# Performance work log

Hardware: AMD Instinct MI355X
Metric: run time of the kernel (lower is better)

The kernel has to match this reference:

```python
import jax, jax.numpy as jnp
import numpy as np

IN_F = 256
OUT_F = 256
ALPHA = 0.2  # LeakyReLU negative slope


def _xavier(key, shape, gain=1.414):
    fan_in, fan_out = shape[0], shape[1]
    limit = gain * np.sqrt(6.0 / (fan_in + fan_out))
    return jax.random.uniform(key, shape, jnp.float32, -limit, limit)


def setup_inputs() -> dict:
    key = jax.random.key(0)
    k1, k2, k3, k4, k5, k6 = jax.random.split(key, 6)
    B, N = 8, 2048
    h = jax.random.normal(k1, (B, N, IN_F), jnp.float32)
    adj = jax.random.randint(k2, (B, N, N), 0, 2, jnp.int32)
    lrgt1 = jax.random.normal(k3, (B, N, OUT_F), jnp.float32)
    W1 = _xavier(k4, (IN_F, IN_F))
    W2 = _xavier(k5, (OUT_F, OUT_F))
    a = _xavier(k6, (2 * IN_F, 1))
    return {"h": h, "adj": adj, "lrgt1": lrgt1, "W1": W1, "W2": W2, "a": a}


def reference(h, adj, lrgt1, W1, W2, a):
    # Wh: [B,N,in], wlrgt: [B,N,out]
    Wh = jnp.matmul(h, W1)
    wlrgt = jnp.matmul(lrgt1, W2)
    # additive attention scores: e[b,i,j] = leaky_relu(Wh_i @ a1 + Wh_j @ a2)
    a1 = a[:IN_F, 0]   # [in]
    a2 = a[IN_F:, 0]   # [in]
    Wh1 = jnp.einsum('bnc,c->bn', Wh, a1)  # [B,N]
    Wh2 = jnp.einsum('bnc,c->bn', Wh, a2)  # [B,N]
    e = jax.nn.leaky_relu(Wh1[:, :, None] + Wh2[:, None, :], ALPHA)  # [B,N,N]
    neg = jnp.float32(-9e15)
    masked = jnp.where(adj > 0, e, neg)
    attention = jax.nn.softmax(masked, axis=2)
    # dropout p=0.0 / eval mode -> identity
    h_prime = jnp.matmul(attention, Wh)      # [B,N,in]
    gt_prime = jnp.matmul(attention, wlrgt)  # [B,N,out]
    return (jax.nn.elu(h_prime), jax.nn.elu(gt_prime))
```

## Files before the change

kernel.cpp:

```cpp
#include <hip/hip_runtime.h>
#include <hip/hip_bf16.h>

#define IN_F 256
#define NN   2048
#define BB   8

typedef unsigned short u16;
typedef unsigned long long u64;
typedef __attribute__((ext_vector_type(8))) short short8x;
typedef __attribute__((ext_vector_type(4))) float float4x;

__device__ __forceinline__ u16 f2b(float f) {
    union { float f; unsigned int u; } x; x.f = f;
    unsigned int r = x.u + 0x7FFFu + ((x.u >> 16) & 1u);
    return (u16)(r >> 16);
}

__global__ __launch_bounds__(256) void adjpack(const int* __restrict__ adj,
                                               u64* __restrict__ mask)
{
    const int wid  = (blockIdx.x * 256 + threadIdx.x) >> 6;
    const int lane = threadIdx.x & 63;
#pragma unroll 4
    for (int it = 0; it < 64; ++it) {
        const long s = (long)it * 8192 + wid;
        const int v = __builtin_nontemporal_load(adj + s * 64 + lane);
        const u64 m = __ballot(v > 0);
        if (lane == 0) mask[s] = m;
    }
}

__device__ __forceinline__ void transp_body4(const float* __restrict__ src,
                                             u16* __restrict__ dst,
                                             int R, int C, int tid,
                                             float (*tile)[33])
{
    const int per = (R / 32) * (C / 32);
    const int b  = tid / per;
    const int tt = tid % per;
    const int jt = tt / (C / 32);
    const int ct = tt % (C / 32);
    src += (long)b * R * C;
    dst += (long)b * R * C;

    const int t = threadIdx.x;
    const int lr = t >> 3, lc = (t & 7) * 4;
    float4 v = *(const float4*)(src + (long)(jt * 32 + lr) * C + ct * 32 + lc);
    tile[lr][lc + 0] = v.x;
    tile[lr][lc + 1] = v.y;
    tile[lr][lc + 2] = v.z;
    tile[lr][lc + 3] = v.w;
    __syncthreads();
    const int c = t >> 3, r4 = (t & 7) * 4;
    ushort4 o;
    o.x = f2b(tile[r4 + 0][c]);
    o.y = f2b(tile[r4 + 1][c]);
    o.z = f2b(tile[r4 + 2][c]);
    o.w = f2b(tile[r4 + 3][c]);
    *(ushort4*)(dst + (long)(ct * 32 + c) * R + jt * 32 + r4) = o;
}

__global__ __launch_bounds__(256) void prep(const float* __restrict__ h,
                                            const float* __restrict__ g,
                                            const float* __restrict__ W1,
                                            const float* __restrict__ W2,
                                            const float* __restrict__ a,
                                            u16* __restrict__ HbfT,
                                            u16* __restrict__ GbfT,
                                            u16* __restrict__ W1T,
                                            u16* __restrict__ W2T,
                                            float* __restrict__ v1,
                                            float* __restrict__ v2)
{
    __shared__ float tile[32][33];
    __shared__ float s1[IN_F], s2[IN_F];
    const int bid = blockIdx.x;

    if (bid < 4096) {
        transp_body4(h, HbfT, NN, IN_F, bid, tile);
    } else if (bid < 8192) {
        transp_body4(g, GbfT, NN, IN_F, bid - 4096, tile);
    } else if (bid < 8256) {
        transp_body4(W1, W1T, IN_F, IN_F, bid - 8192, tile);
    } else if (bid < 8320) {
        transp_body4(W2, W2T, IN_F, IN_F, bid - 8256, tile);
    } else {
        const int t = threadIdx.x;
        s1[t] = a[t];
        s2[t] = a[IN_F + t];
        __syncthreads();
        float acc1 = 0.f, acc2 = 0.f;
        for (int c = 0; c < IN_F; ++c) {
            float w = W1[t * IN_F + c];
            acc1 += w * s1[c];
            acc2 += w * s2[c];
        }
        v1[t] = acc1;
        v2[t] = acc2;
    }
}

__global__ __launch_bounds__(256) void rowdots(const float* __restrict__ h,
                                               const float* __restrict__ v1,
                                               const float* __restrict__ v2,
                                               float* __restrict__ Wh1,
                                               float* __restrict__ Wh2)
{
    const int wave = threadIdx.x >> 6;
    const int lane = threadIdx.x & 63;
    const long row = (long)blockIdx.x * 4 + wave;
    const int c0 = lane * 4;

    float4 v  = *(const float4*)(h + row * IN_F + c0);
    float4 a1 = *(const float4*)(v1 + c0);
    float4 a2 = *(const float4*)(v2 + c0);

    float s1 = v.x * a1.x + v.y * a1.y + v.z * a1.z + v.w * a1.w;
    float s2 = v.x * a2.x + v.y * a2.y + v.z * a2.z + v.w * a2.w;
#pragma unroll
    for (int off = 32; off; off >>= 1) {
        s1 += __shfl_xor(s1, off, 64);
        s2 += __shfl_xor(s2, off, 64);
    }
    if (lane == 0) { Wh1[row] = s1; Wh2[row] = s2; }
}

#define AREAD(AR, KS)                                                         \
    _Pragma("unroll") for (int rt = 0; rt < 4; ++rt)                          \
        AR[rt] = *(const short8x*)&ab[((KS) * 4 + rt) * 512 + lane * 8];

#define MFMA16(AR, G)                                                         \
    _Pragma("unroll") for (int rt = 0; rt < 4; ++rt)                          \
        _Pragma("unroll") for (int ct = 0; ct < 4; ++ct)                      \
            acc[rt][ct] = __builtin_amdgcn_mfma_f32_16x16x32_bf16(AR[rt], G[ct], acc[rt][ct], 0, 0, 0);

#define BISSUE(G, KN, KS)                                                     \
    _Pragma("unroll") for (int ct = 0; ct < 4; ++ct)                          \
        G[ct] = *(const short8x*)(Bp + ct * 16 * NN + ((KN) * 128 + (KS) * 32 + bq8));

#define CHUNK10(KCH, MKC, MKN)                                                \
    {                                                                         \
        const int j0 = (KCH) * 128;                                           \
        const unsigned bits = (MKC) >> ((sg & 1) * 16);                       \
        union { short8x v; u16 e[8]; } pk0, pk1;                              \
        _Pragma("unroll") for (int u = 0; u < 4; ++u) {                       \
            const float4 wv = *(const float4*)&wh2L[j0 + sg * 16 + u * 4];    \
            const float wf[4] = {wv.x, wv.y, wv.z, wv.w};                     \
            _Pragma("unroll") for (int c = 0; c < 4; ++c) {                   \
                float x = wh1rr + wf[c];                                      \
                float ev = fmaxf(x, 0.2f * x);                                \
                float p = __expf(ev - mv);                                    \
                p = ((bits >> (u * 4 + c)) & 1u) ? p : 0.0f;                  \
                lloc += p;                                                    \
                u16 fv = f2b(p);                                              \
                if (u < 2) pk0.e[u * 4 + c] = fv;                             \
                else       pk1.e[(u - 2) * 4 + c] = fv;                       \
            }                                                                 \
        }                                                                     \
        if ((KCH) < 15) MKN = maskR[((KCH) + 1) * 4 + (sg >> 1)];             \
        u16* ab = &Afrag[(KCH) & 1][0];                                       \
        *(short8x*)&ab[wbase0]       = pk0.v;                                 \
        *(short8x*)&ab[wbase0 + 128] = pk1.v;                                 \
        asm volatile("s_waitcnt lgkmcnt(0)\n\ts_barrier" ::: "memory");       \
        AREAD(Aa, 0)                                                          \
        AREAD(Ab, 1)                                                          \
        MFMA16(Aa, G0)                                                        \
        if ((KCH) < 15) { BISSUE(G0, (KCH) + 1, 0) }                          \
        AREAD(Aa, 2)                                                          \
        MFMA16(Ab, G1)                                                        \
        if ((KCH) < 15) { BISSUE(G1, (KCH) + 1, 1) }                          \
        AREAD(Ab, 3)                                                          \
        MFMA16(Aa, G2)                                                        \
        if ((KCH) < 15) { BISSUE(G2, (KCH) + 1, 2) }                          \
        MFMA16(Ab, G3)                                                        \
        if ((KCH) < 15) { BISSUE(G3, (KCH) + 1, 3) }                          \
    }

__global__ __launch_bounds__(512, 2) void attn_mfma(
    const unsigned* __restrict__ mask,
    const u16* __restrict__ HbfT, const u16* __restrict__ GbfT,
    const float* __restrict__ Wh1, const float* __restrict__ Wh2,
    u16* __restrict__ PH, u16* __restrict__ PG)
{
    const int t = threadIdx.x;
    const int wave = t >> 6, lane = t & 63;
    const int bswz = ((blockIdx.x & 7) << 5) | (blockIdx.x >> 3);
    const int b = bswz >> 5;
    const long gi0 = (long)bswz * 64;

    __shared__ __align__(16) u16 Afrag[2][8192];
    __shared__ float wh2L[2048];
    __shared__ float sred[512];
    __shared__ float ssc[65];

    const int rr = t >> 3, sg = t & 7;
    const float* wh2b = Wh2 + (long)b * NN;
    const float wh1rr = Wh1[gi0 + rr];
    const unsigned* maskR = mask + (gi0 + rr) * 64;

    {
        float4 w = *(const float4*)(wh2b + t * 4);
        *(float4*)&wh2L[t * 4] = w;
        sred[t] = fmaxf(fmaxf(w.x, w.y), fmaxf(w.z, w.w));
    }
    __syncthreads();
    if (t < 64) {
        float v = sred[t * 8];
#pragma unroll
        for (int k = 1; k < 8; ++k) v = fmaxf(v, sred[t * 8 + k]);
#pragma unroll
        for (int off = 32; off; off >>= 1) v = fmaxf(v, __shfl_xor(v, off, 64));
        if (t == 0) ssc[64] = v;
    }
    __syncthreads();
    const float mm = wh1rr + ssc[64];
    const float mv = (mm >= 0.f) ? mm : 0.2f * mm;

    const int wbase0 = ((sg >> 1) * 4 + (rr >> 4)) * 512
                     + ((rr & 15) + 16 * (2 * (sg & 1))) * 8;

    float4x acc[4][4];
#pragma unroll
    for (int rt = 0; rt < 4; ++rt)
#pragma unroll
        for (int ct = 0; ct < 4; ++ct) acc[rt][ct] = (float4x)0.0f;

    const int bn = lane & 15, bq = lane >> 4, bq8 = bq * 8;
    const long hbase = (long)b * IN_F * NN;
    const u16* Bp = ((wave < 4) ? HbfT : GbfT) + hbase
                  + (long)((wave & 3) * 64 + bn) * NN;

    float lloc = 0.f;

    short8x Aa[4], Ab[4];
    short8x G0[4], G1[4], G2[4], G3[4];
    unsigned mkA, mkB;

    mkA = maskR[sg >> 1];
    mkB = maskR[4 + (sg >> 1)];
    BISSUE(G0, 0, 0)
    BISSUE(G1, 0, 1)
    BISSUE(G2, 0, 2)
    BISSUE(G3, 0, 3)

    for (int kp = 0; kp < 8; ++kp) {
        CHUNK10(kp * 2,     mkA, mkB)
        CHUNK10(kp * 2 + 1, mkB, mkA)
    }

    sred[t] = lloc;
    __syncthreads();
    if (t < 64) {
        float v = sred[t * 8];
#pragma unroll
        for (int k = 1; k < 8; ++k) v += sred[t * 8 + k];
        ssc[t] = 1.0f / v;
    }
    __syncthreads();

    u16* dst = (wave < 4) ? PH : PG;
    const int colb = (wave & 3) * 64;
#pragma unroll
    for (int rt = 0; rt < 4; ++rt)
#pragma unroll
        for (int ct = 0; ct < 4; ++ct) {
            const int c = colb + ct * 16 + bn;
#pragma unroll
            for (int reg = 0; reg < 4; ++reg) {
                const int rl = rt * 16 + bq * 4 + reg;
                const float il = ssc[rl];
                const long row = gi0 + rl;
                dst[row * IN_F + c] = f2b(acc[rt][ct][reg] * il);
            }
        }
}

#define EPIK(KS, BC, BN_)                                                     \
    {                                                                         \
        if ((KS) < 7) {                                                       \
            _Pragma("unroll") for (int ct = 0; ct < 4; ++ct)                  \
                BN_[ct] = *(const short8x*)(WTrow + ct * 16 * IN_F + ((KS) + 1) * 32 + bq8); \
        }                                                                     \
        short8x A0 = *(const short8x*)&Afrag[(((KS) * 2 + 0) * 64 + lane) * 8]; \
        short8x A1 = *(const short8x*)&Afrag[(((KS) * 2 + 1) * 64 + lane) * 8]; \
        _Pragma("unroll") for (int ct = 0; ct < 4; ++ct) {                    \
            acc[0][ct] = __builtin_amdgcn_mfma_f32_16x16x32_bf16(A0, BC[ct], acc[0][ct], 0, 0, 0); \
            acc[1][ct] = __builtin_amdgcn_mfma_f32_16x16x32_bf16(A1, BC[ct], acc[1][ct], 0, 0, 0); \
        }                                                                     \
    }

__global__ __launch_bounds__(256) void epi2(const u16* __restrict__ PH,
                                            const u16* __restrict__ PG,
                                            const u16* __restrict__ W1T,
                                            const u16* __restrict__ W2T,
                                            float* __restrict__ out)
{
    int bid = blockIdx.x;
    const u16* X;
    const u16* WT;
    float* o;
    if (bid < 512) { X = PH; WT = W1T; o = out; }
    else           { X = PG; WT = W2T; o = out + (long)BB * NN * IN_F; bid -= 512; }

    const int t = threadIdx.x;
    const int wave = t >> 6, lane = t & 63;
    const long i0 = (long)bid * 32;

    __shared__ __align__(16) u16 Afrag[8 * 2 * 64 * 8];

    const int m = t >> 3, ks0 = t & 7, rt0 = m >> 4, lm = m & 15;
    const u16* xp = X + (i0 + m) * IN_F + ks0 * 32;
#pragma unroll
    for (int q = 0; q < 4; ++q) {
        short8x v = *(const short8x*)(xp + q * 8);
        *(short8x*)&Afrag[((ks0 * 2 + rt0) * 64 + lm + q * 16) * 8] = v;
    }

    const int bn = lane & 15, bq = lane >> 4, bq8 = bq * 8;
    const u16* WTrow = WT + (long)(wave * 64 + bn) * IN_F;

    float4x acc[2][4];
#pragma unroll
    for (int rt = 0; rt < 2; ++rt)
#pragma unroll
        for (int ct = 0; ct < 4; ++ct) acc[rt][ct] = (float4x)0.0f;

    short8x BwA[4], BwB[4];
#pragma unroll
    for (int ct = 0; ct < 4; ++ct)
        BwA[ct] = *(const short8x*)(WTrow + ct * 16 * IN_F + bq8);

    __syncthreads();

#pragma unroll
    for (int kp2 = 0; kp2 < 4; ++kp2) {
        EPIK(kp2 * 2,     BwA, BwB)
        EPIK(kp2 * 2 + 1, BwB, BwA)
    }

#pragma unroll
    for (int rt = 0; rt < 2; ++rt)
#pragma unroll
        for (int ct = 0; ct < 4; ++ct) {
            const int n = wave * 64 + ct * 16 + bn;
#pragma unroll
            for (int reg = 0; reg < 4; ++reg) {
                const long row = i0 + rt * 16 + bq * 4 + reg;
                float v = acc[rt][ct][reg];
                v = (v > 0.f) ? v : (__expf(v) - 1.f);
                o[row * IN_F + n] = v;
            }
        }
}

extern "C" void kernel_launch(void* const* d_in, const int* in_sizes, int n_in,
                              void* d_out, int out_size, void* d_ws, size_t ws_size,
                              hipStream_t stream)
{
    int ih = -1, ig = -1, iadj = -1, iw1 = -1, iw2 = -1, ia = -1;
    for (int i = 0; i < n_in; ++i) {
        int s = in_sizes[i];
        if      (s == BB * NN * NN)   { if (iadj < 0) iadj = i; }
        else if (s == BB * NN * IN_F) { if (ih < 0) ih = i; else if (ig < 0) ig = i; }
        else if (s == IN_F * IN_F)    { if (iw1 < 0) iw1 = i; else if (iw2 < 0) iw2 = i; }
        else if (s == 2 * IN_F)       { if (ia < 0) ia = i; }
    }
    if (ih < 0 || ig < 0 || iadj < 0 || iw1 < 0 || iw2 < 0 || ia < 0) {
        ih = 0; iadj = 1; ig = 2; iw1 = 3; iw2 = 4; ia = 5;
    }
    const float* h     = (const float*)d_in[ih];
    const int*   adj   = (const int*)  d_in[iadj];
    const float* lrgt1 = (const float*)d_in[ig];
    const float* W1    = (const float*)d_in[iw1];
    const float* W2    = (const float*)d_in[iw2];
    const float* a     = (const float*)d_in[ia];
    float* out = (float*)d_out;

    u64*      mask64 = (u64*)d_out;
    unsigned* mask32 = (unsigned*)d_out;

    float* ws   = (float*)d_ws;
    float* v1   = ws;
    float* v2   = v1 + IN_F;
    float* Wh1  = v2 + IN_F;
    float* Wh2  = Wh1 + BB * NN;
    u16* W1T  = (u16*)(Wh2 + BB * NN);
    u16* W2T  = W1T + IN_F * IN_F;
    u16* HbfT = W2T + IN_F * IN_F;
    u16* GbfT = HbfT + (long)BB * IN_F * NN;
    u16* PH   = GbfT + (long)BB * IN_F * NN;
    u16* PG   = PH + (long)BB * NN * IN_F;

    const int nrows = BB * NN;

    adjpack  <<<2048,        256, 0, stream>>>(adj, mask64);
    prep     <<<8321,        256, 0, stream>>>(h, lrgt1, W1, W2, a,
                                               HbfT, GbfT, W1T, W2T, v1, v2);
    rowdots  <<<nrows / 4,   256, 0, stream>>>(h, v1, v2, Wh1, Wh2);
    attn_mfma<<<nrows / 64,  512, 0, stream>>>(mask32, HbfT, GbfT, Wh1, Wh2, PH, PG);
    epi2     <<<2 * nrows / 32, 256, 0, stream>>>(PH, PG, W1T, W2T, out);
}
```

Baseline: 335.9 us.

## Fuse adjacency bit-packing into attention kernel prologue via shared memory

Removes the separate adjpack kernel and instead has each attention block read its 64 rows of the int32 adjacency matrix directly. It packs them into 16-bit masks in shared memory, and the chunk loop reads those masks from LDS instead of global memory. This saves a kernel launch and the round trip of the packed mask through global memory. The cost is a large serial load phase at the start of each block before any MFMA work, plus extra LDS use, which could lower occupancy and leave the 512MB adjacency read poorly overlapped with compute.

```diff
diff --git a/kernel.cpp b/kernel.cpp
--- a/kernel.cpp
+++ b/kernel.cpp
@@ -14,20 +14,6 @@
     union { float f; unsigned int u; } x; x.f = f;
     unsigned int r = x.u + 0x7FFFu + ((x.u >> 16) & 1u);
     return (u16)(r >> 16);
-}
-
-__global__ __launch_bounds__(256) void adjpack(const int* __restrict__ adj,
-                                               u64* __restrict__ mask)
-{
-    const int wid  = (blockIdx.x * 256 + threadIdx.x) >> 6;
-    const int lane = threadIdx.x & 63;
-#pragma unroll 4
-    for (int it = 0; it < 64; ++it) {
-        const long s = (long)it * 8192 + wid;
-        const int v = __builtin_nontemporal_load(adj + s * 64 + lane);
-        const u64 m = __ballot(v > 0);
-        if (lane == 0) mask[s] = m;
-    }
 }
 
 __device__ __forceinline__ void transp_body4(const float* __restrict__ src,
@@ -138,10 +124,10 @@
     _Pragma("unroll") for (int ct = 0; ct < 4; ++ct)                          \
         G[ct] = *(const short8x*)(Bp + ct * 16 * NN + ((KN) * 128 + (KS) * 32 + bq8));
 
-#define CHUNK10(KCH, MKC, MKN)                                                \
+#define CHUNK11(KCH, MKC, MKN)                                                \
     {                                                                         \
         const int j0 = (KCH) * 128;                                           \
-        const unsigned bits = (MKC) >> ((sg & 1) * 16);                       \
+        const unsigned bits = (MKC);                                          \
         union { short8x v; u16 e[8]; } pk0, pk1;                              \
         _Pragma("unroll") for (int u = 0; u < 4; ++u) {                       \
             const float4 wv = *(const float4*)&wh2L[j0 + sg * 16 + u * 4];    \
@@ -157,7 +143,7 @@
                 else       pk1.e[(u - 2) * 4 + c] = fv;                       \
             }                                                                 \
         }                                                                     \
-        if ((KCH) < 15) MKN = maskR[((KCH) + 1) * 4 + (sg >> 1)];             \
+        if ((KCH) < 15) MKN = maskL[mrow + ((KCH) + 1) * 8 + sg];             \
         u16* ab = &Afrag[(KCH) & 1][0];                                       \
         *(short8x*)&ab[wbase0]       = pk0.v;                                 \
         *(short8x*)&ab[wbase0 + 128] = pk1.v;                                 \
@@ -177,7 +163,7 @@
     }
 
 __global__ __launch_bounds__(512, 2) void attn_mfma(
-    const unsigned* __restrict__ mask,
+    const int* __restrict__ adj,
     const u16* __restrict__ HbfT, const u16* __restrict__ GbfT,
     const float* __restrict__ Wh1, const float* __restrict__ Wh2,
     u16* __restrict__ PH, u16* __restrict__ PG)
@@ -190,19 +176,43 @@
 
     __shared__ __align__(16) u16 Afrag[2][8192];
     __shared__ float wh2L[2048];
+    __shared__ u16 maskL[8192];
     __shared__ float sred[512];
     __shared__ float ssc[65];
 
     const int rr = t >> 3, sg = t & 7;
     const float* wh2b = Wh2 + (long)b * NN;
     const float wh1rr = Wh1[gi0 + rr];
-    const unsigned* maskR = mask + (gi0 + rr) * 64;
+    const int mrow = rr * 128;
 
     {
         float4 w = *(const float4*)(wh2b + t * 4);
         *(float4*)&wh2L[t * 4] = w;
         sred[t] = fmaxf(fmaxf(w.x, w.y), fmaxf(w.z, w.w));
     }
+
+    {
+        const int* adjB = adj + gi0 * (long)NN;
+#pragma unroll 4
+        for (int it = 0; it < 16; ++it) {
+            const int s = it * 512 + t;
+            const int4* p4 = (const int4*)(adjB + (long)s * 16);
+            const int4 v0 = p4[0];
+            const int4 v1 = p4[1];
+            const int4 v2 = p4[2];
+            const int4 v3 = p4[3];
+            unsigned m = 0;
+            m |= ((unsigned)(v0.x > 0))       | ((unsigned)(v0.y > 0) << 1)
+               | ((unsigned)(v0.z > 0) << 2)  | ((unsigned)(v0.w > 0) << 3)
+               | ((unsigned)(v1.x > 0) << 4)  | ((unsigned)(v1.y > 0) << 5)
+               | ((unsigned)(v1.z > 0) << 6)  | ((unsigned)(v1.w > 0) << 7)
+               | ((unsigned)(v2.x > 0) << 8)  | ((unsigned)(v2.y > 0) << 9)
+               | ((unsigned)(v2.z > 0) << 10) | ((unsigned)(v2.w > 0) << 11)
+               | ((unsigned)(v3.x > 0) << 12) | ((unsigned)(v3.y > 0) << 13)
+               | ((unsigned)(v3.z > 0) << 14) | ((unsigned)(v3.w > 0) << 15);
+            maskL[s] = (u16)m;
+        }
+    }
     __syncthreads();
     if (t < 64) {
         float v = sred[t * 8];
@@ -236,16 +246,16 @@
     short8x G0[4], G1[4], G2[4], G3[4];
     unsigned mkA, mkB;
 
-    mkA = maskR[sg >> 1];
-    mkB = maskR[4 + (sg >> 1)];
+    mkA = maskL[mrow + sg];
+    mkB = maskL[mrow + 8 + sg];
     BISSUE(G0, 0, 0)
     BISSUE(G1, 0, 1)
     BISSUE(G2, 0, 2)
     BISSUE(G3, 0, 3)
 
     for (int kp = 0; kp < 8; ++kp) {
-        CHUNK10(kp * 2,     mkA, mkB)
-        CHUNK10(kp * 2 + 1, mkB, mkA)
+        CHUNK11(kp * 2,     mkA, mkB)
+        CHUNK11(kp * 2 + 1, mkB, mkA)
     }
 
     sred[t] = lloc;
@@ -376,9 +386,6 @@
     const float* a     = (const float*)d_in[ia];
     float* out = (float*)d_out;
 
-    u64*      mask64 = (u64*)d_out;
-    unsigned* mask32 = (unsigned*)d_out;
-
     float* ws   = (float*)d_ws;
     float* v1   = ws;
     float* v2   = v1 + IN_F;
@@ -393,10 +400,9 @@
 
     const int nrows = BB * NN;
 
-    adjpack  <<<2048,        256, 0, stream>>>(adj, mask64);
     prep     <<<8321,        256, 0, stream>>>(h, lrgt1, W1, W2, a,
                                                HbfT, GbfT, W1T, W2T, v1, v2);
     rowdots  <<<nrows / 4,   256, 0, stream>>>(h, v1, v2, Wh1, Wh2);
-    attn_mfma<<<nrows / 64,  512, 0, stream>>>(mask32, HbfT, GbfT, Wh1, Wh2, PH, PG);
+    attn_mfma<<<nrows / 64,  512, 0, stream>>>(adj, HbfT, GbfT, Wh1, Wh2, PH, PG);
     epi2     <<<2 * nrows / 32, 256, 0, stream>>>(PH, PG, W1T, W2T, out);
 }
```

Result: faster. 323.6 us (-3.7%).
